# Performance work log

Measured on AMD Instinct MI355X. Metric: run time of the kernel, lower is better.

The kernel has to match this reference:

```python
import jax, jax.numpy as jnp
import numpy as np
from jax import lax

B, S, D, L, HID = 256, 512, 64, 64, 256  # batch, seq_len, input_dim, latent_dim, MLP hidden


def setup_inputs() -> dict:
    key = jax.random.key(0)
    ks = jax.random.split(key, 16)
    sc = 0.05  # small init scale for MLP weights

    def eye_noise(k, n):
        # identity init (as in nn.Parameter(torch.eye)) plus small noise so inverse is non-trivial
        return jnp.eye(n, dtype=jnp.float32) + 0.05 * jax.random.normal(k, (n, n), dtype=jnp.float32)

    return {
        "x": jax.random.normal(ks[0], (B, S, D), dtype=jnp.float32),
        "eps": jax.random.normal(ks[1], (B, S, L), dtype=jnp.float32),
        "enc_w1": sc * jax.random.normal(ks[2], (D, HID), dtype=jnp.float32),
        "enc_b1": jnp.zeros((HID,), dtype=jnp.float32),
        "enc_w2": sc * jax.random.normal(ks[3], (HID, 2 * L), dtype=jnp.float32),
        "enc_b2": jnp.zeros((2 * L,), dtype=jnp.float32),
        "dec_w1": sc * jax.random.normal(ks[4], (L, HID), dtype=jnp.float32),
        "dec_b1": jnp.zeros((HID,), dtype=jnp.float32),
        "dec_w2": sc * jax.random.normal(ks[5], (HID, D), dtype=jnp.float32),
        "dec_b2": jnp.zeros((D,), dtype=jnp.float32),
        "A": eye_noise(ks[6], L),   # transition_matrix
        "Q": eye_noise(ks[7], L),   # process_covariance
        "Hm": eye_noise(ks[8], L),  # measurement_matrix
        "R": eye_noise(ks[9], L),   # measurement_covariance
    }


def reference(x, eps, enc_w1, enc_b1, enc_w2, enc_b2,
              dec_w1, dec_b1, dec_w2, dec_b2, A, Q, Hm, R):
    Bb, Ss, _ = x.shape
    # ---- encoder on all timesteps at once (no temporal dependency) ----
    h = jax.nn.relu(jnp.einsum('bsd,dh->bsh', x, enc_w1) + enc_b1)
    ml = jnp.einsum('bsh,hk->bsk', h, enc_w2) + enc_b2          # [B,S,2L]
    z_mean, z_logvar = jnp.split(ml, 2, axis=-1)                 # [B,S,L] each
    z = z_mean + eps * jnp.exp(0.5 * z_logvar)                   # reparameterize

    # ---- Kalman recursion; covariances don't depend on state in source, hoist ----
    AQ = A @ Q                                                   # z_pred_cov
    innov_cov = Hm @ AQ + R
    K = AQ @ jnp.linalg.inv(innov_cov)                           # kalman gain [L,L]

    def step(z_prev, inputs):
        x_t, z_t = inputs                                        # [B,D], [B,L]
        z_pred = z_prev @ A.T + z_t                              # (A @ z_prev^T)^T + z
        innovation = x_t - z_pred @ Hm.T
        z_up = z_pred + innovation @ K.T
        return z_up, z_up

    xs = (jnp.swapaxes(x, 0, 1), jnp.swapaxes(z, 0, 1))          # time-major [S,B,*]
    z0 = jnp.zeros((Bb, L), dtype=x.dtype)
    _, z_upd = lax.scan(step, z0, xs)                            # [S,B,L]
    z_upd = jnp.swapaxes(z_upd, 0, 1)                            # [B,S,L]

    # ---- decoder ----
    hd = jax.nn.relu(jnp.einsum('bsl,lh->bsh', z_upd, dec_w1) + dec_b1)
    x_recon = jax.nn.sigmoid(jnp.einsum('bsh,hd->bsd', hd, dec_w2) + dec_b2)

    return x_recon, z_mean.reshape(-1, L), z_logvar.reshape(-1, L)
```

## Files before the change

kernel.cpp:

```cpp
#include <hip/hip_runtime.h>
#include <hip/hip_bf16.h>


typedef short short8 __attribute__((ext_vector_type(8)));
typedef float f32x4 __attribute__((ext_vector_type(4)));

#define NROW 131072
#define OUTSEG 8388608

__device__ __forceinline__ unsigned short f2bf(float f) {
    unsigned int u = __builtin_bit_cast(unsigned int, f);
    u += 0x7fffu + ((u >> 16) & 1u);
    return (unsigned short)(u >> 16);
}
__device__ __forceinline__ float bf2f(unsigned short h) {
    unsigned int u = ((unsigned int)h) << 16;
    return __builtin_bit_cast(float, u);
}

__device__ void mm64(const float* A, int lda, const float* B, int ldb,
                     float* C, int ldc, int mode, const float* Add, int ldadd,
                     int tid) {
    int i = tid & 63;
    int j0 = (tid >> 6) * 8;
    float acc[8];
#pragma unroll
    for (int jj = 0; jj < 8; jj++) acc[jj] = 0.f;
    for (int k = 0; k < 64; k++) {
        float a = A[i * lda + k];
#pragma unroll
        for (int jj = 0; jj < 8; jj++) acc[jj] += a * B[k * ldb + j0 + jj];
    }
#pragma unroll
    for (int jj = 0; jj < 8; jj++) {
        int j = j0 + jj;
        float v = acc[jj];
        if (mode == 1) v += Add[i * ldadd + j];
        if (mode == 2) v = ((i == j) ? 1.f : 0.f) - v;
        C[i * ldc + j] = v;
    }
}

__device__ void load64(const float* g, float* L, int tid) {
    for (int idx = tid; idx < 4096; idx += 512)
        L[(idx >> 6) * 65 + (idx & 63)] = g[idx];
}

__global__ __launch_bounds__(512) void kprep(
    const float* __restrict__ Ain, const float* __restrict__ Qin,
    const float* __restrict__ Hin, const float* __restrict__ Rin,
    const float* __restrict__ ew1, const float* __restrict__ ew2,
    const float* __restrict__ dw1, const float* __restrict__ dw2,
    float* __restrict__ Mw, unsigned short* __restrict__ Gb,
    unsigned short* __restrict__ Kb, unsigned short* __restrict__ w1t,
    unsigned short* __restrict__ w2t, unsigned short* __restrict__ d1t,
    unsigned short* __restrict__ d2t) {
    __shared__ float La[64 * 65], Lb[64 * 65], Lc[64 * 65];
    __shared__ float aug[64 * 129];
    __shared__ int pividx;
    __shared__ float pivval;
    int tid = threadIdx.x;

    load64(Ain, La, tid);
    load64(Qin, Lb, tid);
    __syncthreads();
    mm64(La, 65, Lb, 65, Lc, 65, 0, nullptr, 0, tid);
    __syncthreads();
    load64(Hin, La, tid);
    load64(Rin, Lb, tid);
    __syncthreads();
    mm64(La, 65, Lc, 65, aug, 129, 1, Lb, 65, tid);
    for (int idx = tid; idx < 4096; idx += 512) {
        int i = idx >> 6, j = idx & 63;
        aug[i * 129 + 64 + j] = (i == j) ? 1.f : 0.f;
    }
    __syncthreads();

    for (int k = 0; k < 64; k++) {
        if (tid < 64) {
            float v = (tid >= k) ? fabsf(aug[tid * 129 + k]) : -1.f;
            int ix = tid;
#pragma unroll
            for (int off = 1; off < 64; off <<= 1) {
                float ov = __shfl_xor(v, off);
                int oi = __shfl_xor(ix, off);
                if (ov > v) { v = ov; ix = oi; }
            }
            if (tid == 0) { pividx = ix; pivval = aug[ix * 129 + k]; }
        }
        __syncthreads();
        int p = pividx;
        float rp = 1.0f / pivval;
        if (p != k) {
            if (tid < 128) {
                float t1 = aug[k * 129 + tid];
                aug[k * 129 + tid] = aug[p * 129 + tid];
                aug[p * 129 + tid] = t1;
            }
            __syncthreads();
        }
        int i = tid & 63;
        float mlt = (i != k) ? aug[i * 129 + k] : 0.f;
        if (tid < 128) aug[k * 129 + tid] *= rp;
        __syncthreads();
        int j0 = (tid >> 6) * 16;
        if (i != k) {
#pragma unroll
            for (int jj = 0; jj < 16; jj++) {
                int j = j0 + jj;
                aug[i * 129 + j] -= mlt * aug[k * 129 + j];
            }
        }
        __syncthreads();
    }

    mm64(Lc, 65, aug + 64, 129, Lb, 65, 0, nullptr, 0, tid);
    __syncthreads();
    mm64(Lb, 65, La, 65, Lc, 65, 2, nullptr, 0, tid);
    __syncthreads();
    for (int idx = tid; idx < 4096; idx += 512) {
        int i = idx >> 6, j = idx & 63;
        Kb[idx] = f2bf(Lb[i * 65 + j]);
        Gb[idx] = f2bf(Lc[i * 65 + j]);
    }
    load64(Ain, La, tid);
    __syncthreads();
    mm64(Lc, 65, La, 65, aug, 129, 0, nullptr, 0, tid);
    __syncthreads();
    for (int idx = tid; idx < 4096; idx += 512)
        Mw[idx] = aug[(idx >> 6) * 129 + (idx & 63)];

    for (int idx = tid; idx < 256 * 64; idx += 512) {
        int h = idx >> 6, d = idx & 63;
        w1t[idx] = f2bf(ew1[d * 256 + h]);
    }
    for (int idx = tid; idx < 128 * 256; idx += 512) {
        int o = idx >> 8, h = idx & 255;
        w2t[idx] = f2bf(ew2[h * 128 + o]);
    }
    for (int idx = tid; idx < 256 * 64; idx += 512) {
        int h = idx >> 6, l = idx & 63;
        d1t[idx] = f2bf(dw1[l * 256 + h]);
    }
    for (int idx = tid; idx < 64 * 256; idx += 512) {
        int d = idx >> 8, h = idx & 255;
        d2t[idx] = f2bf(dw2[h * 64 + d]);
    }
}

__global__ __launch_bounds__(256) void kenc(
    const float* __restrict__ x, const float* __restrict__ eps,
    const float* __restrict__ b1, const float* __restrict__ b2,
    const unsigned short* __restrict__ w1t, const unsigned short* __restrict__ w2t,
    const unsigned short* __restrict__ Gb, const unsigned short* __restrict__ Kb,
    unsigned short* __restrict__ cbuf, float* __restrict__ zmean,
    float* __restrict__ zlogv) {
    __shared__ unsigned short Xs[64][72];
    __shared__ unsigned short Hs[64][264];
    __shared__ unsigned short Zs[64][72];
    int row0 = blockIdx.x * 64;
    int tid = threadIdx.x;
    int lane = tid & 63, w = tid >> 6;
    int ml = lane & 15, kg = lane >> 4;

    {
        int r = tid >> 2, c0 = (tid & 3) * 16;
        const float4* xp = reinterpret_cast<const float4*>(&x[(size_t)(row0 + r) * 64 + c0]);
        float4 v0 = xp[0], v1 = xp[1], v2 = xp[2], v3 = xp[3];
        short8 s0, s1;
        s0[0] = (short)f2bf(v0.x); s0[1] = (short)f2bf(v0.y);
        s0[2] = (short)f2bf(v0.z); s0[3] = (short)f2bf(v0.w);
        s0[4] = (short)f2bf(v1.x); s0[5] = (short)f2bf(v1.y);
        s0[6] = (short)f2bf(v1.z); s0[7] = (short)f2bf(v1.w);
        s1[0] = (short)f2bf(v2.x); s1[1] = (short)f2bf(v2.y);
        s1[2] = (short)f2bf(v2.z); s1[3] = (short)f2bf(v2.w);
        s1[4] = (short)f2bf(v3.x); s1[5] = (short)f2bf(v3.y);
        s1[6] = (short)f2bf(v3.z); s1[7] = (short)f2bf(v3.w);
        *reinterpret_cast<short8*>(&Xs[r][c0]) = s0;
        *reinterpret_cast<short8*>(&Xs[r][c0 + 8]) = s1;
    }
    __syncthreads();

    short8 afr[4][2];
#pragma unroll
    for (int mt = 0; mt < 4; mt++)
#pragma unroll
        for (int kb = 0; kb < 2; kb++)
            afr[mt][kb] = *reinterpret_cast<const short8*>(&Xs[mt * 16 + ml][kb * 32 + kg * 8]);

#pragma unroll
    for (int q = 0; q < 4; q++) {
        int nt = w * 4 + q;
        f32x4 acc[4];
#pragma unroll
        for (int mt = 0; mt < 4; mt++) acc[mt] = (f32x4){0.f, 0.f, 0.f, 0.f};
#pragma unroll
        for (int kb = 0; kb < 2; kb++) {
            short8 bfr = *reinterpret_cast<const short8*>(&w1t[(nt * 16 + ml) * 64 + kb * 32 + kg * 8]);
#pragma unroll
            for (int mt = 0; mt < 4; mt++)
                acc[mt] = __builtin_amdgcn_mfma_f32_16x16x32_bf16(afr[mt][kb], bfr, acc[mt], 0, 0, 0);
        }
        float bias = b1[nt * 16 + ml];
#pragma unroll
        for (int mt = 0; mt < 4; mt++)
#pragma unroll
            for (int i = 0; i < 4; i++) {
                float v = acc[mt][i] + bias;
                v = v > 0.f ? v : 0.f;
                Hs[mt * 16 + kg * 4 + i][nt * 16 + ml] = f2bf(v);
            }
    }
    __syncthreads();

    f32x4 acc2[2][4];
#pragma unroll
    for (int p = 0; p < 2; p++)
#pragma unroll
        for (int mt = 0; mt < 4; mt++) acc2[p][mt] = (f32x4){0.f, 0.f, 0.f, 0.f};
#pragma unroll
    for (int kb = 0; kb < 8; kb++) {
        short8 a2[4];
#pragma unroll
        for (int mt = 0; mt < 4; mt++)
            a2[mt] = *reinterpret_cast<const short8*>(&Hs[mt * 16 + ml][kb * 32 + kg * 8]);
#pragma unroll
        for (int p = 0; p < 2; p++) {
            int nt = w + 4 * p;
            short8 bfr = *reinterpret_cast<const short8*>(&w2t[(nt * 16 + ml) * 256 + kb * 32 + kg * 8]);
#pragma unroll
            for (int mt = 0; mt < 4; mt++)
                acc2[p][mt] = __builtin_amdgcn_mfma_f32_16x16x32_bf16(a2[mt], bfr, acc2[p][mt], 0, 0, 0);
        }
    }
    int colz = w * 16 + ml;
    float bm = b2[colz], bl = b2[64 + colz];
#pragma unroll
    for (int mt = 0; mt < 4; mt++)
#pragma unroll
        for (int i = 0; i < 4; i++) {
            int r = mt * 16 + kg * 4 + i;
            size_t grow = (size_t)(row0 + r);
            float zm = acc2[0][mt][i] + bm;
            float zl = acc2[1][mt][i] + bl;
            zmean[grow * 64 + colz] = zm;
            zlogv[grow * 64 + colz] = zl;
            float zz = zm + eps[grow * 64 + colz] * expf(0.5f * zl);
            Zs[r][colz] = f2bf(zz);
        }
    __syncthreads();

    f32x4 acc3[4];
#pragma unroll
    for (int mt = 0; mt < 4; mt++) acc3[mt] = (f32x4){0.f, 0.f, 0.f, 0.f};
    short8 az[4][2];
#pragma unroll
    for (int mt = 0; mt < 4; mt++)
#pragma unroll
        for (int kb = 0; kb < 2; kb++)
            az[mt][kb] = *reinterpret_cast<const short8*>(&Zs[mt * 16 + ml][kb * 32 + kg * 8]);
#pragma unroll
    for (int kb = 0; kb < 2; kb++) {
        short8 bg = *reinterpret_cast<const short8*>(&Gb[(w * 16 + ml) * 64 + kb * 32 + kg * 8]);
        short8 bk = *reinterpret_cast<const short8*>(&Kb[(w * 16 + ml) * 64 + kb * 32 + kg * 8]);
#pragma unroll
        for (int mt = 0; mt < 4; mt++)
            acc3[mt] = __builtin_amdgcn_mfma_f32_16x16x32_bf16(az[mt][kb], bg, acc3[mt], 0, 0, 0);
#pragma unroll
        for (int mt = 0; mt < 4; mt++)
            acc3[mt] = __builtin_amdgcn_mfma_f32_16x16x32_bf16(afr[mt][kb], bk, acc3[mt], 0, 0, 0);
    }
#pragma unroll
    for (int mt = 0; mt < 4; mt++)
#pragma unroll
        for (int i = 0; i < 4; i++) {
            int r = mt * 16 + kg * 4 + i;
            cbuf[(size_t)(row0 + r) * 64 + colz] = f2bf(acc3[mt][i]);
        }
}

__global__ __launch_bounds__(256) void kscan(const float* __restrict__ Mw,
                                             const unsigned short* __restrict__ cbuf,
                                             float* __restrict__ zu) {
    __shared__ float zs[2][64];
    int b = blockIdx.x, tid = threadIdx.x;
    int j = tid >> 2, g = tid & 3;
    float m[16];
#pragma unroll
    for (int i = 0; i < 16; i++) m[i] = Mw[j * 64 + g * 16 + i];
    if (tid < 128) ((float*)zs)[tid] = 0.f;
    const unsigned short* cb = cbuf + (size_t)b * 512 * 64;
    float* zo = zu + (size_t)b * 512 * 64;
    float cval = bf2f(cb[j]);
    __syncthreads();
    int cur = 0;
    for (int t = 0; t < 512; ++t) {
        unsigned short unext = (t < 511) ? cb[(t + 1) * 64 + j] : (unsigned short)0;
        const float4* zp = reinterpret_cast<const float4*>(&zs[cur][g * 16]);
        float4 z0 = zp[0], z1 = zp[1], z2 = zp[2], z3 = zp[3];
        float pa = m[0] * z0.x + m[1] * z0.y + m[2] * z0.z + m[3] * z0.w;
        float pb = m[4] * z1.x + m[5] * z1.y + m[6] * z1.z + m[7] * z1.w;
        pa += m[8] * z2.x + m[9] * z2.y + m[10] * z2.z + m[11] * z2.w;
        pb += m[12] * z3.x + m[13] * z3.y + m[14] * z3.z + m[15] * z3.w;
        float part = pa + pb;
        part += __shfl_xor(part, 1);
        part += __shfl_xor(part, 2);
        float z = cval + part;
        if (g == 0) {
            zs[cur ^ 1][j] = z;
            zo[(size_t)t * 64 + j] = z;
        }
        cval = bf2f(unext);
        cur ^= 1;
        __syncthreads();
    }
}

__global__ __launch_bounds__(256) void kdec(float* __restrict__ xr,
                                            const float* __restrict__ db1,
                                            const float* __restrict__ db2,
                                            const unsigned short* __restrict__ d1t,
                                            const unsigned short* __restrict__ d2t) {
    __shared__ unsigned short Zs[64][72];
    __shared__ unsigned short Hs[64][264];
    int row0 = blockIdx.x * 64;
    int tid = threadIdx.x;
    int lane = tid & 63, w = tid >> 6;
    int ml = lane & 15, kg = lane >> 4;

    {
        int r = tid >> 2, c0 = (tid & 3) * 16;
        const float4* zp = reinterpret_cast<const float4*>(&xr[(size_t)(row0 + r) * 64 + c0]);
        float4 v0 = zp[0], v1 = zp[1], v2 = zp[2], v3 = zp[3];
        short8 s0, s1;
        s0[0] = (short)f2bf(v0.x); s0[1] = (short)f2bf(v0.y);
        s0[2] = (short)f2bf(v0.z); s0[3] = (short)f2bf(v0.w);
        s0[4] = (short)f2bf(v1.x); s0[5] = (short)f2bf(v1.y);
        s0[6] = (short)f2bf(v1.z); s0[7] = (short)f2bf(v1.w);
        s1[0] = (short)f2bf(v2.x); s1[1] = (short)f2bf(v2.y);
        s1[2] = (short)f2bf(v2.z); s1[3] = (short)f2bf(v2.w);
        s1[4] = (short)f2bf(v3.x); s1[5] = (short)f2bf(v3.y);
        s1[6] = (short)f2bf(v3.z); s1[7] = (short)f2bf(v3.w);
        *reinterpret_cast<short8*>(&Zs[r][c0]) = s0;
        *reinterpret_cast<short8*>(&Zs[r][c0 + 8]) = s1;
    }
    __syncthreads();

    short8 afr[4][2];
#pragma unroll
    for (int mt = 0; mt < 4; mt++)
#pragma unroll
        for (int kb = 0; kb < 2; kb++)
            afr[mt][kb] = *reinterpret_cast<const short8*>(&Zs[mt * 16 + ml][kb * 32 + kg * 8]);

#pragma unroll
    for (int q = 0; q < 4; q++) {
        int nt = w * 4 + q;
        f32x4 acc[4];
#pragma unroll
        for (int mt = 0; mt < 4; mt++) acc[mt] = (f32x4){0.f, 0.f, 0.f, 0.f};
#pragma unroll
        for (int kb = 0; kb < 2; kb++) {
            short8 bfr = *reinterpret_cast<const short8*>(&d1t[(nt * 16 + ml) * 64 + kb * 32 + kg * 8]);
#pragma unroll
            for (int mt = 0; mt < 4; mt++)
                acc[mt] = __builtin_amdgcn_mfma_f32_16x16x32_bf16(afr[mt][kb], bfr, acc[mt], 0, 0, 0);
        }
        float bias = db1[nt * 16 + ml];
#pragma unroll
        for (int mt = 0; mt < 4; mt++)
#pragma unroll
            for (int i = 0; i < 4; i++) {
                float v = acc[mt][i] + bias;
                v = v > 0.f ? v : 0.f;
                Hs[mt * 16 + kg * 4 + i][nt * 16 + ml] = f2bf(v);
            }
    }
    __syncthreads();

    f32x4 acc2[4];
#pragma unroll
    for (int mt = 0; mt < 4; mt++) acc2[mt] = (f32x4){0.f, 0.f, 0.f, 0.f};
#pragma unroll
    for (int kb = 0; kb < 8; kb++) {
        short8 bfr = *reinterpret_cast<const short8*>(&d2t[(w * 16 + ml) * 256 + kb * 32 + kg * 8]);
#pragma unroll
        for (int mt = 0; mt < 4; mt++) {
            short8 a2 = *reinterpret_cast<const short8*>(&Hs[mt * 16 + ml][kb * 32 + kg * 8]);
            acc2[mt] = __builtin_amdgcn_mfma_f32_16x16x32_bf16(a2, bfr, acc2[mt], 0, 0, 0);
        }
    }
    float bias2 = db2[w * 16 + ml];
#pragma unroll
    for (int mt = 0; mt < 4; mt++)
#pragma unroll
        for (int i = 0; i < 4; i++) {
            int r = mt * 16 + kg * 4 + i;
            float v = acc2[mt][i] + bias2;
            float s = 1.f / (1.f + expf(-v));
            xr[(size_t)(row0 + r) * 64 + w * 16 + ml] = s;
        }
}

extern "C" void kernel_launch(void* const* d_in, const int* in_sizes, int n_in,
                              void* d_out, int out_size, void* d_ws, size_t ws_size,
                              hipStream_t stream) {
    (void)in_sizes; (void)n_in; (void)out_size; (void)ws_size;
    const float* x      = (const float*)d_in[0];
    const float* eps    = (const float*)d_in[1];
    const float* enc_w1 = (const float*)d_in[2];
    const float* enc_b1 = (const float*)d_in[3];
    const float* enc_w2 = (const float*)d_in[4];
    const float* enc_b2 = (const float*)d_in[5];
    const float* dec_w1 = (const float*)d_in[6];
    const float* dec_b1 = (const float*)d_in[7];
    const float* dec_w2 = (const float*)d_in[8];
    const float* dec_b2 = (const float*)d_in[9];
    const float* Ain    = (const float*)d_in[10];
    const float* Qin    = (const float*)d_in[11];
    const float* Hin    = (const float*)d_in[12];
    const float* Rin    = (const float*)d_in[13];

    float* out   = (float*)d_out;
    float* xrec  = out;
    float* zmean = out + OUTSEG;
    float* zlogv = out + 2 * OUTSEG;

    char* ws = (char*)d_ws;
    float*          Mw   = (float*)(ws);
    unsigned short* Gb   = (unsigned short*)(ws + 16384);
    unsigned short* Kb   = (unsigned short*)(ws + 24576);
    unsigned short* w1t  = (unsigned short*)(ws + 32768);
    unsigned short* w2t  = (unsigned short*)(ws + 65536);
    unsigned short* d1t  = (unsigned short*)(ws + 131072);
    unsigned short* d2t  = (unsigned short*)(ws + 163840);
    unsigned short* cbuf = (unsigned short*)(ws + 196608);

    hipLaunchKernelGGL(kprep, dim3(1), dim3(512), 0, stream,
                       Ain, Qin, Hin, Rin, enc_w1, enc_w2, dec_w1, dec_w2,
                       Mw, Gb, Kb, w1t, w2t, d1t, d2t);
    hipLaunchKernelGGL(kenc, dim3(2048), dim3(256), 0, stream,
                       x, eps, enc_b1, enc_b2, w1t, w2t, Gb, Kb, cbuf, zmean, zlogv);
    hipLaunchKernelGGL(kscan, dim3(256), dim3(256), 0, stream, Mw, cbuf, xrec);
    hipLaunchKernelGGL(kdec, dim3(2048), dim3(256), 0, stream,
                       xrec, dec_b1, dec_b2, d1t, d2t);
}
```

Before: 507.7 us.

## Replace sequential Kalman scan with chunked parallel scan using M^16 carry chain

The 512-step per-batch serial scan is replaced by a three-phase chunked linear scan. The encoder computes each 16-step chunk's local recurrence with readlane matvecs. A small kernel chains the chunk carries using M^16, which is precomputed by repeated squaring in kprep. The decoder then recomputes each chunk's states from its carry-in before the MLP. Weight transposes in kprep are also spread across extra blocks as tiled transposes, and the Gauss-Jordan step is restructured. The cost is redundant matvec work and some error from chaining carries through M^16 in fp32 with bf16 inputs.

Result: faster. 424.2 us (-16.4%).

```diff
diff --git a/kernel.cpp b/kernel.cpp
--- a/kernel.cpp
+++ b/kernel.cpp
@@ -5,7 +5,6 @@
 typedef short short8 __attribute__((ext_vector_type(8)));
 typedef float f32x4 __attribute__((ext_vector_type(4)));
 
-#define NROW 131072
 #define OUTSEG 8388608
 
 __device__ __forceinline__ unsigned short f2bf(float f) {
@@ -17,22 +16,44 @@
     unsigned int u = ((unsigned int)h) << 16;
     return __builtin_bit_cast(float, u);
 }
+__device__ __forceinline__ float rlf(float v, int l) {
+    return __builtin_bit_cast(float, __builtin_amdgcn_readlane(__builtin_bit_cast(int, v), l));
+}
+__device__ __forceinline__ float matvec_rl(const float* m, float z, float c) {
+    float a0 = c, a1 = 0.f, a2 = 0.f, a3 = 0.f;
+#pragma unroll
+    for (int k = 0; k < 64; k += 4) {
+        a0 = fmaf(m[k + 0], rlf(z, k + 0), a0);
+        a1 = fmaf(m[k + 1], rlf(z, k + 1), a1);
+        a2 = fmaf(m[k + 2], rlf(z, k + 2), a2);
+        a3 = fmaf(m[k + 3], rlf(z, k + 3), a3);
+    }
+    return (a0 + a1) + (a2 + a3);
+}
+__device__ __forceinline__ void load_mrow(const float* Mp, int j, float* m) {
+#pragma unroll
+    for (int q = 0; q < 16; q++) {
+        float4 v = *reinterpret_cast<const float4*>(&Mp[j * 64 + q * 4]);
+        m[q * 4 + 0] = v.x; m[q * 4 + 1] = v.y;
+        m[q * 4 + 2] = v.z; m[q * 4 + 3] = v.w;
+    }
+}
 
 __device__ void mm64(const float* A, int lda, const float* B, int ldb,
                      float* C, int ldc, int mode, const float* Add, int ldadd,
                      int tid) {
     int i = tid & 63;
-    int j0 = (tid >> 6) * 8;
-    float acc[8];
-#pragma unroll
-    for (int jj = 0; jj < 8; jj++) acc[jj] = 0.f;
+    int j0 = (tid >> 6) * 16;
+    float acc[16];
+#pragma unroll
+    for (int jj = 0; jj < 16; jj++) acc[jj] = 0.f;
     for (int k = 0; k < 64; k++) {
         float a = A[i * lda + k];
 #pragma unroll
-        for (int jj = 0; jj < 8; jj++) acc[jj] += a * B[k * ldb + j0 + jj];
-    }
-#pragma unroll
-    for (int jj = 0; jj < 8; jj++) {
+        for (int jj = 0; jj < 16; jj++) acc[jj] += a * B[k * ldb + j0 + jj];
+    }
+#pragma unroll
+    for (int jj = 0; jj < 16; jj++) {
         int j = j0 + jj;
         float v = acc[jj];
         if (mode == 1) v += Add[i * ldadd + j];
@@ -42,24 +63,57 @@
 }
 
 __device__ void load64(const float* g, float* L, int tid) {
-    for (int idx = tid; idx < 4096; idx += 512)
+    for (int idx = tid; idx < 4096; idx += 256)
         L[(idx >> 6) * 65 + (idx & 63)] = g[idx];
 }
 
-__global__ __launch_bounds__(512) void kprep(
+__device__ void tr_tile(const float* src, int sld, unsigned short* dst, int dld,
+                        int r0, int c0, int tid, float* LT) {
+    int rr = tid >> 2, q = tid & 3;
+#pragma unroll
+    for (int u = 0; u < 4; u++) {
+        float4 v = *reinterpret_cast<const float4*>(
+            &src[(size_t)(r0 + rr) * sld + c0 + q * 16 + u * 4]);
+        LT[rr * 65 + q * 16 + u * 4 + 0] = v.x;
+        LT[rr * 65 + q * 16 + u * 4 + 1] = v.y;
+        LT[rr * 65 + q * 16 + u * 4 + 2] = v.z;
+        LT[rr * 65 + q * 16 + u * 4 + 3] = v.w;
+    }
+    __syncthreads();
+    short8 s0, s1;
+#pragma unroll
+    for (int u = 0; u < 8; u++) s0[u] = (short)f2bf(LT[(q * 16 + u) * 65 + rr]);
+#pragma unroll
+    for (int u = 0; u < 8; u++) s1[u] = (short)f2bf(LT[(q * 16 + 8 + u) * 65 + rr]);
+    *reinterpret_cast<short8*>(&dst[(size_t)(c0 + rr) * dld + r0 + q * 16]) = s0;
+    *reinterpret_cast<short8*>(&dst[(size_t)(c0 + rr) * dld + r0 + q * 16 + 8]) = s1;
+}
+
+__global__ __launch_bounds__(256) void kprep(
     const float* __restrict__ Ain, const float* __restrict__ Qin,
     const float* __restrict__ Hin, const float* __restrict__ Rin,
     const float* __restrict__ ew1, const float* __restrict__ ew2,
     const float* __restrict__ dw1, const float* __restrict__ dw2,
-    float* __restrict__ Mw, unsigned short* __restrict__ Gb,
-    unsigned short* __restrict__ Kb, unsigned short* __restrict__ w1t,
-    unsigned short* __restrict__ w2t, unsigned short* __restrict__ d1t,
-    unsigned short* __restrict__ d2t) {
+    float* __restrict__ Mw, float* __restrict__ M16w,
+    unsigned short* __restrict__ Gb, unsigned short* __restrict__ Kb,
+    unsigned short* __restrict__ w1t, unsigned short* __restrict__ w2t,
+    unsigned short* __restrict__ d1t, unsigned short* __restrict__ d2t) {
     __shared__ float La[64 * 65], Lb[64 * 65], Lc[64 * 65];
     __shared__ float aug[64 * 129];
-    __shared__ int pividx;
-    __shared__ float pivval;
+    __shared__ int s_piv;
+    __shared__ float s_pv;
     int tid = threadIdx.x;
+
+    if (blockIdx.x != 0) {
+        int t = blockIdx.x - 1;
+        const float* src; unsigned short* dst; int sld, dld, r0, c0;
+        if (t < 4)       { src = ew1; dst = w1t; sld = 256; dld = 64;  r0 = 0;             c0 = t * 64; }
+        else if (t < 12) { int i = t - 4;  src = ew2; dst = w2t; sld = 128; dld = 256; r0 = (i >> 1) * 64; c0 = (i & 1) * 64; }
+        else if (t < 16) { int i = t - 12; src = dw1; dst = d1t; sld = 256; dld = 64;  r0 = 0;             c0 = i * 64; }
+        else             { int i = t - 16; src = dw2; dst = d2t; sld = 64;  dld = 256; r0 = i * 64;        c0 = 0; }
+        tr_tile(src, sld, dst, dld, r0, c0, tid, La);
+        return;
+    }
 
     load64(Ain, La, tid);
     load64(Qin, Lb, tid);
@@ -70,7 +124,7 @@
     load64(Rin, Lb, tid);
     __syncthreads();
     mm64(La, 65, Lc, 65, aug, 129, 1, Lb, 65, tid);
-    for (int idx = tid; idx < 4096; idx += 512) {
+    for (int idx = tid; idx < 4096; idx += 256) {
         int i = idx >> 6, j = idx & 63;
         aug[i * 129 + 64 + j] = (i == j) ? 1.f : 0.f;
     }
@@ -86,30 +140,32 @@
                 int oi = __shfl_xor(ix, off);
                 if (ov > v) { v = ov; ix = oi; }
             }
-            if (tid == 0) { pividx = ix; pivval = aug[ix * 129 + k]; }
+            if (tid == 0) { s_piv = ix; s_pv = aug[ix * 129 + k]; }
         }
         __syncthreads();
-        int p = pividx;
-        float rp = 1.0f / pivval;
+        int p = s_piv;
+        float rp = 1.0f / s_pv;
         if (p != k) {
-            if (tid < 128) {
-                float t1 = aug[k * 129 + tid];
-                aug[k * 129 + tid] = aug[p * 129 + tid];
-                aug[p * 129 + tid] = t1;
+            for (int idx = tid; idx < 129; idx += 256) {
+                float t1 = aug[k * 129 + idx];
+                aug[k * 129 + idx] = aug[p * 129 + idx];
+                aug[p * 129 + idx] = t1;
             }
             __syncthreads();
         }
-        int i = tid & 63;
-        float mlt = (i != k) ? aug[i * 129 + k] : 0.f;
-        if (tid < 128) aug[k * 129 + tid] *= rp;
+        int i = tid & 63, jb = tid >> 6;
+        float mlt = aug[i * 129 + k] * rp;
+        float pv[33], rw[33];
+#pragma unroll
+        for (int jj = 0; jj < 33; jj++) {
+            int j = jb + 4 * jj;
+            if (j < 129) { pv[jj] = aug[k * 129 + j]; rw[jj] = aug[i * 129 + j]; }
+        }
         __syncthreads();
-        int j0 = (tid >> 6) * 16;
-        if (i != k) {
-#pragma unroll
-            for (int jj = 0; jj < 16; jj++) {
-                int j = j0 + jj;
-                aug[i * 129 + j] -= mlt * aug[k * 129 + j];
-            }
+#pragma unroll
+        for (int jj = 0; jj < 33; jj++) {
+            int j = jb + 4 * jj;
+            if (j < 129) aug[i * 129 + j] = (i == k) ? pv[jj] * rp : rw[jj] - mlt * pv[jj];
         }
         __syncthreads();
     }
@@ -118,7 +174,7 @@
     __syncthreads();
     mm64(Lb, 65, La, 65, Lc, 65, 2, nullptr, 0, tid);
     __syncthreads();
-    for (int idx = tid; idx < 4096; idx += 512) {
+    for (int idx = tid; idx < 4096; idx += 256) {
         int i = idx >> 6, j = idx & 63;
         Kb[idx] = f2bf(Lb[i * 65 + j]);
         Gb[idx] = f2bf(Lc[i * 65 + j]);
@@ -127,25 +183,19 @@
     __syncthreads();
     mm64(Lc, 65, La, 65, aug, 129, 0, nullptr, 0, tid);
     __syncthreads();
-    for (int idx = tid; idx < 4096; idx += 512)
+    for (int idx = tid; idx < 4096; idx += 256)
         Mw[idx] = aug[(idx >> 6) * 129 + (idx & 63)];
-
-    for (int idx = tid; idx < 256 * 64; idx += 512) {
-        int h = idx >> 6, d = idx & 63;
-        w1t[idx] = f2bf(ew1[d * 256 + h]);
-    }
-    for (int idx = tid; idx < 128 * 256; idx += 512) {
-        int o = idx >> 8, h = idx & 255;
-        w2t[idx] = f2bf(ew2[h * 128 + o]);
-    }
-    for (int idx = tid; idx < 256 * 64; idx += 512) {
-        int h = idx >> 6, l = idx & 63;
-        d1t[idx] = f2bf(dw1[l * 256 + h]);
-    }
-    for (int idx = tid; idx < 64 * 256; idx += 512) {
-        int d = idx >> 8, h = idx & 255;
-        d2t[idx] = f2bf(dw2[h * 64 + d]);
-    }
+    __syncthreads();
+    mm64(aug, 129, aug, 129, Lb, 65, 0, nullptr, 0, tid);
+    __syncthreads();
+    mm64(Lb, 65, Lb, 65, Lc, 65, 0, nullptr, 0, tid);
+    __syncthreads();
+    mm64(Lc, 65, Lc, 65, La, 65, 0, nullptr, 0, tid);
+    __syncthreads();
+    mm64(La, 65, La, 65, Lb, 65, 0, nullptr, 0, tid);
+    __syncthreads();
+    for (int idx = tid; idx < 4096; idx += 256)
+        M16w[idx] = Lb[(idx >> 6) * 65 + (idx & 63)];
 }
 
 __global__ __launch_bounds__(256) void kenc(
@@ -153,7 +203,8 @@
     const float* __restrict__ b1, const float* __restrict__ b2,
     const unsigned short* __restrict__ w1t, const unsigned short* __restrict__ w2t,
     const unsigned short* __restrict__ Gb, const unsigned short* __restrict__ Kb,
-    unsigned short* __restrict__ cbuf, float* __restrict__ zmean,
+    const float* __restrict__ Mw, unsigned short* __restrict__ cbuf,
+    float* __restrict__ Pbuf, float* __restrict__ zmean,
     float* __restrict__ zlogv) {
     __shared__ unsigned short Xs[64][72];
     __shared__ unsigned short Hs[64][264];
@@ -273,46 +324,47 @@
 #pragma unroll
     for (int mt = 0; mt < 4; mt++)
 #pragma unroll
-        for (int i = 0; i < 4; i++) {
-            int r = mt * 16 + kg * 4 + i;
-            cbuf[(size_t)(row0 + r) * 64 + colz] = f2bf(acc3[mt][i]);
-        }
-}
-
-__global__ __launch_bounds__(256) void kscan(const float* __restrict__ Mw,
-                                             const unsigned short* __restrict__ cbuf,
-                                             float* __restrict__ zu) {
-    __shared__ float zs[2][64];
-    int b = blockIdx.x, tid = threadIdx.x;
-    int j = tid >> 2, g = tid & 3;
-    float m[16];
-#pragma unroll
-    for (int i = 0; i < 16; i++) m[i] = Mw[j * 64 + g * 16 + i];
-    if (tid < 128) ((float*)zs)[tid] = 0.f;
-    const unsigned short* cb = cbuf + (size_t)b * 512 * 64;
-    float* zo = zu + (size_t)b * 512 * 64;
-    float cval = bf2f(cb[j]);
-    __syncthreads();
-    int cur = 0;
-    for (int t = 0; t < 512; ++t) {
-        unsigned short unext = (t < 511) ? cb[(t + 1) * 64 + j] : (unsigned short)0;
-        const float4* zp = reinterpret_cast<const float4*>(&zs[cur][g * 16]);
-        float4 z0 = zp[0], z1 = zp[1], z2 = zp[2], z3 = zp[3];
-        float pa = m[0] * z0.x + m[1] * z0.y + m[2] * z0.z + m[3] * z0.w;
-        float pb = m[4] * z1.x + m[5] * z1.y + m[6] * z1.z + m[7] * z1.w;
-        pa += m[8] * z2.x + m[9] * z2.y + m[10] * z2.z + m[11] * z2.w;
-        pb += m[12] * z3.x + m[13] * z3.y + m[14] * z3.z + m[15] * z3.w;
-        float part = pa + pb;
-        part += __shfl_xor(part, 1);
-        part += __shfl_xor(part, 2);
-        float z = cval + part;
-        if (g == 0) {
-            zs[cur ^ 1][j] = z;
-            zo[(size_t)t * 64 + j] = z;
-        }
-        cval = bf2f(unext);
-        cur ^= 1;
-        __syncthreads();
+        for (int i = 0; i < 4; i++)
+            Xs[mt * 16 + kg * 4 + i][colz] = f2bf(acc3[mt][i]);
+    __syncthreads();
+
+    {
+        int r = tid >> 2, c0 = (tid & 3) * 16;
+        short8 s0 = *reinterpret_cast<const short8*>(&Xs[r][c0]);
+        short8 s1 = *reinterpret_cast<const short8*>(&Xs[r][c0 + 8]);
+        *reinterpret_cast<short8*>(&cbuf[(size_t)(row0 + r) * 64 + c0]) = s0;
+        *reinterpret_cast<short8*>(&cbuf[(size_t)(row0 + r) * 64 + c0 + 8]) = s1;
+    }
+
+    {
+        int j = lane;
+        float m[64];
+        load_mrow(Mw, j, m);
+        unsigned short cv[16];
+#pragma unroll
+        for (int t = 0; t < 16; t++) cv[t] = Xs[w * 16 + t][j];
+        float z = bf2f(cv[0]);
+#pragma unroll
+        for (int t = 1; t < 16; t++) z = matvec_rl(m, z, bf2f(cv[t]));
+        int b = row0 >> 9;
+        int chunk = ((row0 & 511) >> 4) + w;
+        if (chunk != 31)
+            Pbuf[((size_t)b * 32 + chunk + 1) * 64 + j] = z;
+    }
+}
+
+__global__ __launch_bounds__(64) void kchain(const float* __restrict__ M16w,
+                                             float* __restrict__ Pbuf) {
+    int b = blockIdx.x, j = threadIdx.x;
+    float m[64];
+    load_mrow(M16w, j, m);
+    float* P = Pbuf + (size_t)b * 32 * 64;
+    P[j] = 0.f;
+    float z = 0.f;
+    for (int c = 1; c < 32; c++) {
+        float f = P[c * 64 + j];
+        z = matvec_rl(m, z, f);
+        P[c * 64 + j] = z;
     }
 }
 
@@ -320,7 +372,10 @@
                                             const float* __restrict__ db1,
                                             const float* __restrict__ db2,
                                             const unsigned short* __restrict__ d1t,
-                                            const unsigned short* __restrict__ d2t) {
+                                            const unsigned short* __restrict__ d2t,
+                                            const float* __restrict__ Mw,
+                                            const float* __restrict__ Pbuf,
+                                            const unsigned short* __restrict__ cbuf) {
     __shared__ unsigned short Zs[64][72];
     __shared__ unsigned short Hs[64][264];
     int row0 = blockIdx.x * 64;
@@ -329,20 +384,21 @@
     int ml = lane & 15, kg = lane >> 4;
 
     {
-        int r = tid >> 2, c0 = (tid & 3) * 16;
-        const float4* zp = reinterpret_cast<const float4*>(&xr[(size_t)(row0 + r) * 64 + c0]);
-        float4 v0 = zp[0], v1 = zp[1], v2 = zp[2], v3 = zp[3];
-        short8 s0, s1;
-        s0[0] = (short)f2bf(v0.x); s0[1] = (short)f2bf(v0.y);
-        s0[2] = (short)f2bf(v0.z); s0[3] = (short)f2bf(v0.w);
-        s0[4] = (short)f2bf(v1.x); s0[5] = (short)f2bf(v1.y);
-        s0[6] = (short)f2bf(v1.z); s0[7] = (short)f2bf(v1.w);
-        s1[0] = (short)f2bf(v2.x); s1[1] = (short)f2bf(v2.y);
-        s1[2] = (short)f2bf(v2.z); s1[3] = (short)f2bf(v2.w);
-        s1[4] = (short)f2bf(v3.x); s1[5] = (short)f2bf(v3.y);
-        s1[6] = (short)f2bf(v3.z); s1[7] = (short)f2bf(v3.w);
-        *reinterpret_cast<short8*>(&Zs[r][c0]) = s0;
-        *reinterpret_cast<short8*>(&Zs[r][c0 + 8]) = s1;
+        int j = lane;
+        int b = row0 >> 9;
+        int chunk = ((row0 & 511) >> 4) + w;
+        float m[64];
+        load_mrow(Mw, j, m);
+        float z = Pbuf[((size_t)b * 32 + chunk) * 64 + j];
+        const unsigned short* cb = cbuf + ((size_t)row0 + w * 16) * 64;
+        unsigned short cv[16];
+#pragma unroll
+        for (int t = 0; t < 16; t++) cv[t] = cb[t * 64 + j];
+#pragma unroll
+        for (int t = 0; t < 16; t++) {
+            z = matvec_rl(m, z, bf2f(cv[t]));
+            Zs[w * 16 + t][j] = f2bf(z);
+        }
     }
     __syncthreads();
 
@@ -428,20 +484,23 @@
 
     char* ws = (char*)d_ws;
     float*          Mw   = (float*)(ws);
-    unsigned short* Gb   = (unsigned short*)(ws + 16384);
-    unsigned short* Kb   = (unsigned short*)(ws + 24576);
-    unsigned short* w1t  = (unsigned short*)(ws + 32768);
-    unsigned short* w2t  = (unsigned short*)(ws + 65536);
-    unsigned short* d1t  = (unsigned short*)(ws + 131072);
-    unsigned short* d2t  = (unsigned short*)(ws + 163840);
-    unsigned short* cbuf = (unsigned short*)(ws + 196608);
-
-    hipLaunchKernelGGL(kprep, dim3(1), dim3(512), 0, stream,
+    float*          M16w = (float*)(ws + 16384);
+    unsigned short* Gb   = (unsigned short*)(ws + 32768);
+    unsigned short* Kb   = (unsigned short*)(ws + 40960);
+    unsigned short* w1t  = (unsigned short*)(ws + 49152);
+    unsigned short* w2t  = (unsigned short*)(ws + 81920);
+    unsigned short* d1t  = (unsigned short*)(ws + 147456);
+    unsigned short* d2t  = (unsigned short*)(ws + 180224);
+    float*          Pbuf = (float*)(ws + 212992);
+    unsigned short* cbuf = (unsigned short*)(ws + 2310144);
+
+    hipLaunchKernelGGL(kprep, dim3(21), dim3(256), 0, stream,
                        Ain, Qin, Hin, Rin, enc_w1, enc_w2, dec_w1, dec_w2,
-                       Mw, Gb, Kb, w1t, w2t, d1t, d2t);
+                       Mw, M16w, Gb, Kb, w1t, w2t, d1t, d2t);
     hipLaunchKernelGGL(kenc, dim3(2048), dim3(256), 0, stream,
-                       x, eps, enc_b1, enc_b2, w1t, w2t, Gb, Kb, cbuf, zmean, zlogv);
-    hipLaunchKernelGGL(kscan, dim3(256), dim3(256), 0, stream, Mw, cbuf, xrec);
+                       x, eps, enc_b1, enc_b2, w1t, w2t, Gb, Kb, Mw, cbuf, Pbuf,
+                       zmean, zlogv);
+    hipLaunchKernelGGL(kchain, dim3(256), dim3(64), 0, stream, M16w, Pbuf);
     hipLaunchKernelGGL(kdec, dim3(2048), dim3(256), 0, stream,
-                       xrec, dec_b1, dec_b2, d1t, d2t);
-}
+                       xrec, dec_b1, dec_b2, d1t, d2t, Mw, Pbuf, cbuf);
+}
```
